# Kernel tuning notes

Measured on AMD Instinct MI355X. Metric: run time of the kernel, lower is better.

## Reference

```python
import jax, jax.numpy as jnp
import numpy as np

DIM = 128
G = 2
N = G * G * G
EPS = 1e-5


def _positions():
    pos = []
    for x in range(G):
        for y in range(G):
            for z in range(G):
                pos.append([x / (G - 1), y / (G - 1), z / (G - 1)])
    return np.asarray(pos, dtype=np.float32)  # [N, 3]


def _nearby(idx):
    x = idx // (G * G)
    y = (idx % (G * G)) // G
    z = idx % G
    nb = []
    for dx in (-1, 0, 1):
        for dy in (-1, 0, 1):
            for dz in (-1, 0, 1):
                nx, ny, nz = x + dx, y + dy, z + dz
                if 0 <= nx < G and 0 <= ny < G and 0 <= nz < G:
                    nidx = nx * G * G + ny * G + nz
                    if nidx != idx:
                        nb.append(nidx)
    return nb


def _ln(h, g, b):
    m = h.mean(-1, keepdims=True)
    v = ((h - m) ** 2).mean(-1, keepdims=True)
    return (h - m) * jax.lax.rsqrt(v + EPS) * g + b


def setup_inputs() -> dict:
    key = jax.random.key(0)
    ks = jax.random.split(key, 16)
    B = 131072
    f32 = jnp.float32
    return {
        "x": jax.random.normal(ks[0], (B, DIM), f32),
        "field_basis": jax.random.normal(ks[1], (N, 8, DIM), f32) * 0.02,
        "spatial_mix": jax.random.normal(ks[2], (N, 3, DIM), f32) * 0.02,
        "ln1_g": jnp.ones((N, DIM), f32),
        "ln1_b": jnp.zeros((N, DIM), f32),
        "w1": jax.random.normal(ks[3], (N, DIM, 2 * DIM), f32) * 0.02,
        "b1": jnp.zeros((N, 2 * DIM), f32),
        "w2": jax.random.normal(ks[4], (N, 2 * DIM, DIM), f32) * 0.02,
        "b2": jnp.zeros((N, DIM), f32),
        "ln2_g": jnp.ones((N, DIM), f32),
        "ln2_b": jnp.zeros((N, DIM), f32),
        "comb_ln_g": jnp.ones((DIM,), f32),
        "comb_ln_b": jnp.zeros((DIM,), f32),
        "comb_w": jax.random.normal(ks[5], (DIM, DIM), f32) * 0.02,
        "comb_b": jnp.zeros((DIM,), f32),
    }


def reference(x, field_basis, spatial_mix, ln1_g, ln1_b, w1, b1, w2, b2,
              ln2_g, ln2_b, comb_ln_g, comb_ln_b, comb_w, comb_b):
    pos = jnp.asarray(_positions())  # [N, 3] constant grid positions
    states = []
    for i in range(N):
        # per-module field value
        pw = jax.nn.sigmoid(pos[i] @ spatial_mix[i])          # [dim]
        fv = (field_basis[i] * pw).mean(0)                     # [dim]
        # neighbor contribution: only previously computed modules (j < i)
        nbrs = [j for j in _nearby(i) if j < i]
        h = x + fv
        if nbrs:
            nc = 0.1 * jnp.mean(jnp.stack([states[j] for j in nbrs], 0), 0)
            h = h + nc
        # LN -> Linear(dim,2dim) -> GELU(exact) -> Linear(2dim,dim) -> LN
        h = _ln(h, ln1_g[i], ln1_b[i])
        h = jax.nn.gelu(h @ w1[i] + b1[i], approximate=False)
        h = h @ w2[i] + b2[i]
        h = _ln(h, ln2_g[i], ln2_b[i])
        states.append(h)
    s = jnp.stack(states, 1).mean(1)                           # [B, dim]
    return _ln(s, comb_ln_g, comb_ln_b) @ comb_w + comb_b
```

## Files before the change

kernel.cpp:

```cpp
#include <hip/hip_runtime.h>
#include <math.h>


#define NMOD 8

typedef float    f32x4  __attribute__((ext_vector_type(4)));
typedef _Float16 f16x8  __attribute__((ext_vector_type(8)));
typedef _Float16 f16x2  __attribute__((ext_vector_type(2)));
typedef __fp16   fp16v2 __attribute__((ext_vector_type(2)));

union PKC { fp16v2 raw; f16x2 v; };
static __device__ __forceinline__ f16x2 pkrtz(float a, float b) {
    PKC u; u.raw = __builtin_amdgcn_cvt_pkrtz(a, b); return u.v;
}

union U16V { f16x8 v; f16x2 p[4]; };

#define AHI_OFF 0u
#define ALO_OFF 8192u
#define HHI_OFF 16384u
#define HLO_OFF 24576u

#define WS_W1 0u
#define WS_W2 1048576u
#define WS_CW 2097152u
#define WS_FV 2162688u

#define WSCALE 64.0f
#define INV64  0.015625f

static __device__ __forceinline__ float gelu_fast(float y) {
    float z  = y * 0.70710678118654752440f;
    float az = fabsf(z);
    float t  = __builtin_amdgcn_rcpf(1.0f + 0.3275911f * az);
    float poly = t * (0.254829592f + t * (-0.284496736f + t * (1.421413741f
               + t * (-1.453152027f + t * 1.061405429f))));
    float e  = __expf(-az * az);
    float erfa = 1.0f - poly * e;
    float er = (z < 0.0f) ? -erfa : erfa;
    return 0.5f * y * (1.0f + er);
}

#define MFMA16(a, b, c) __builtin_amdgcn_mfma_f32_16x16x32_f16((a), (b), (c), 0, 0, 0)

__global__ void setup_weights(const float* __restrict__ w1,
                              const float* __restrict__ w2,
                              const float* __restrict__ cw,
                              _Float16* __restrict__ w1cv,
                              _Float16* __restrict__ w2cv,
                              _Float16* __restrict__ cwcv)
{
    unsigned id = blockIdx.x * blockDim.x + threadIdx.x;
    if (id < 262144u) {
        unsigned i8 = id & 7u;
        unsigned l  = (id >> 3) & 63u;
        unsigned nt = (id >> 9) & 15u;
        unsigned ks = (id >> 13) & 3u;
        unsigned mo = id >> 15;
        unsigned k = ks * 32u + ((l >> 4) << 3) + i8;
        unsigned c = nt * 16u + (l & 15u);
        float v = w1[(mo * 128u + k) * 256u + c] * WSCALE;
        _Float16 hh = (_Float16)v;
        _Float16 ll = (_Float16)(v - (float)hh);
        w1cv[((((mo * 2u + 0u) * 4u + ks) * 16u + nt) * 64u + l) * 8u + i8] = hh;
        w1cv[((((mo * 2u + 1u) * 4u + ks) * 16u + nt) * 64u + l) * 8u + i8] = ll;
    } else if (id < 524288u) {
        unsigned id2 = id - 262144u;
        unsigned i8 = id2 & 7u;
        unsigned l  = (id2 >> 3) & 63u;
        unsigned nt = (id2 >> 9) & 7u;
        unsigned kt = (id2 >> 12) & 7u;
        unsigned mo = id2 >> 15;
        unsigned k = kt * 32u + ((l >> 4) << 3) + i8;
        unsigned c = nt * 16u + (l & 15u);
        float v = w2[(mo * 256u + k) * 128u + c] * WSCALE;
        _Float16 hh = (_Float16)v;
        _Float16 ll = (_Float16)(v - (float)hh);
        w2cv[((((mo * 2u + 0u) * 8u + kt) * 8u + nt) * 64u + l) * 8u + i8] = hh;
        w2cv[((((mo * 2u + 1u) * 8u + kt) * 8u + nt) * 64u + l) * 8u + i8] = ll;
    } else if (id < 540672u) {
        unsigned id3 = id - 524288u;
        unsigned i8 = id3 & 7u;
        unsigned l  = (id3 >> 3) & 63u;
        unsigned nt = (id3 >> 9) & 7u;
        unsigned ks = id3 >> 12;
        unsigned k = ks * 32u + ((l >> 4) << 3) + i8;
        unsigned c = nt * 16u + (l & 15u);
        float v = cw[k * 128u + c] * WSCALE;
        _Float16 hh = (_Float16)v;
        _Float16 ll = (_Float16)(v - (float)hh);
        cwcv[(((0u * 4u + ks) * 8u + nt) * 64u + l) * 8u + i8] = hh;
        cwcv[(((1u * 4u + ks) * 8u + nt) * 64u + l) * 8u + i8] = ll;
    }
}

__global__ void setup_fv(const float* __restrict__ fb,
                         const float* __restrict__ sm,
                         float* __restrict__ fv)
{
    unsigned tid = blockIdx.x * blockDim.x + threadIdx.x;
    unsigned i = tid >> 7, d = tid & 127u;
    float px = (float)((i >> 2) & 1u);
    float py = (float)((i >> 1) & 1u);
    float pz = (float)(i & 1u);
    float dot = px * sm[(i * 3u + 0u) * 128u + d]
              + py * sm[(i * 3u + 1u) * 128u + d]
              + pz * sm[(i * 3u + 2u) * 128u + d];
    float pw = 1.0f / (1.0f + expf(-dot));
    float mb = 0.0f;
    #pragma unroll
    for (int k = 0; k < 8; ++k) mb += fb[(i * 8u + (unsigned)k) * 128u + d];
    mb *= 0.125f;
    fv[i * 128u + d] = pw * mb;
}

__global__ __launch_bounds__(256)
__attribute__((amdgpu_waves_per_eu(3, 4)))
void holo_main(const float* __restrict__ x,
               const float* __restrict__ ln1_g, const float* __restrict__ ln1_b,
               const float* __restrict__ bias1, const float* __restrict__ bias2,
               const float* __restrict__ ln2_g, const float* __restrict__ ln2_b,
               const float* __restrict__ cln_g, const float* __restrict__ cln_b,
               const float* __restrict__ comb_b,
               const _Float16* __restrict__ w1cv,
               const _Float16* __restrict__ w2cv,
               const _Float16* __restrict__ cwcv,
               const float* __restrict__ fv,
               float* __restrict__ out)
{
    __shared__ __align__(16) unsigned char lds[32768];

    const unsigned t  = threadIdx.x;
    const unsigned r  = t >> 3;
    const unsigned q8 = t & 7u;
    const unsigned w  = t >> 6;
    const unsigned l  = t & 63u;
    const unsigned lr = l & 15u;
    const unsigned lg = l >> 4;
    const unsigned drow = lg * 4u;
    const unsigned row0 = blockIdx.x * 32u;

    const f32x4 FZ = {0.f, 0.f, 0.f, 0.f};

    float Sv[16];
    #pragma unroll
    for (int j = 0; j < 16; ++j) Sv[j] = 0.f;

    for (int mod = 0; mod < NMOD; ++mod) {
        const unsigned mo = (unsigned)mod;
        {
            const float coef = (mod == 0) ? 0.0f : (0.1f / (float)mod);
            float h[16];
            const float4* xp  = (const float4*)(x  + (row0 + r) * 128u + q8 * 16u);
            const float4* fvp = (const float4*)(fv + mo * 128u + q8 * 16u);
            #pragma unroll
            for (int u = 0; u < 4; ++u) {
                float4 xv = xp[u];
                float4 f4 = fvp[u];
                h[4*u+0] = xv.x + f4.x + coef * Sv[4*u+0];
                h[4*u+1] = xv.y + f4.y + coef * Sv[4*u+1];
                h[4*u+2] = xv.z + f4.z + coef * Sv[4*u+2];
                h[4*u+3] = xv.w + f4.w + coef * Sv[4*u+3];
            }
            float s = 0.f;
            #pragma unroll
            for (int j = 0; j < 16; ++j) s += h[j];
            s += __shfl_xor(s, 1); s += __shfl_xor(s, 2); s += __shfl_xor(s, 4);
            const float mean = s * (1.0f / 128.0f);
            float ss = 0.f;
            #pragma unroll
            for (int j = 0; j < 16; ++j) { float d = h[j] - mean; ss += d * d; }
            ss += __shfl_xor(ss, 1); ss += __shfl_xor(ss, 2); ss += __shfl_xor(ss, 4);
            const float var  = ss * (1.0f / 128.0f);
            const float rstd = 1.0f / sqrtf(var + 1e-5f);
            const float4* gp = (const float4*)(ln1_g + mo * 128u + q8 * 16u);
            const float4* bp = (const float4*)(ln1_b + mo * 128u + q8 * 16u);
            #pragma unroll
            for (int e2 = 0; e2 < 2; ++e2) {
                U16V vh, vl;
                #pragma unroll
                for (int u = 0; u < 2; ++u) {
                    float4 g4 = gp[e2*2+u], b4 = bp[e2*2+u];
                    int e0 = e2*8 + u*4;
                    float n0 = (h[e0+0] - mean) * rstd * g4.x + b4.x;
                    float n1 = (h[e0+1] - mean) * rstd * g4.y + b4.y;
                    float n2 = (h[e0+2] - mean) * rstd * g4.z + b4.z;
                    float n3 = (h[e0+3] - mean) * rstd * g4.w + b4.w;
                    f16x2 h01 = pkrtz(n0, n1);
                    f16x2 h23 = pkrtz(n2, n3);
                    f16x2 l01 = pkrtz(n0 - (float)h01[0], n1 - (float)h01[1]);
                    f16x2 l23 = pkrtz(n2 - (float)h23[0], n3 - (float)h23[1]);
                    vh.p[u*2+0] = h01; vh.p[u*2+1] = h23;
                    vl.p[u*2+0] = l01; vl.p[u*2+1] = l23;
                }
                unsigned off = ((r * 256u + q8 * 32u + (unsigned)e2 * 16u) ^ ((r & 7u) << 4));
                *(f16x8*)(lds + AHI_OFF + off) = vh.v;
                *(f16x8*)(lds + ALO_OFF + off) = vl.v;
            }
        }
        __syncthreads();

        f32x4 acc2[2][2];
        #pragma unroll
        for (int m = 0; m < 2; ++m) { acc2[m][0] = FZ; acc2[m][1] = FZ; }

        #pragma unroll
        for (int hN = 0; hN < 2; ++hN) {
            if (hN == 1) __syncthreads();
            #pragma unroll
            for (int n = 0; n < 2; ++n) {
                f32x4 a1[2];
                a1[0] = FZ; a1[1] = FZ;
                #pragma unroll
                for (int ks = 0; ks < 4; ++ks) {
                    f16x8 ah[2], al[2];
                    #pragma unroll
                    for (int m = 0; m < 2; ++m) {
                        unsigned rowA = (unsigned)m * 16u + lr;
                        unsigned off = ((rowA * 256u + (unsigned)ks * 64u + lg * 16u) ^ ((lr & 7u) << 4));
                        ah[m] = *(const f16x8*)(lds + AHI_OFF + off);
                        al[m] = *(const f16x8*)(lds + ALO_OFF + off);
                    }
                    unsigned ntg = (unsigned)hN * 8u + w * 2u + (unsigned)n;
                    const f16x8 bh = *(const f16x8*)(const void*)
                        (w1cv + (((mo * 2u + 0u) * 4u + (unsigned)ks) * 16u + ntg) * 512u + l * 8u);
                    const f16x8 bl = *(const f16x8*)(const void*)
                        (w1cv + (((mo * 2u + 1u) * 4u + (unsigned)ks) * 16u + ntg) * 512u + l * 8u);
                    #pragma unroll
                    for (int m = 0; m < 2; ++m) {
                        a1[m] = MFMA16(ah[m], bh, a1[m]);
                        a1[m] = MFMA16(al[m], bh, a1[m]);
                        a1[m] = MFMA16(ah[m], bl, a1[m]);
                    }
                }
                unsigned c128 = w * 32u + (unsigned)n * 16u + lr;
                float bb = bias1[mo * 256u + (unsigned)hN * 128u + c128];
                #pragma unroll
                for (int m = 0; m < 2; ++m) {
                    float ge[4];
                    #pragma unroll
                    for (int j = 0; j < 4; ++j)
                        ge[j] = gelu_fast(a1[m][j] * INV64 + bb);
                    f16x2 h01 = pkrtz(ge[0], ge[1]);
                    f16x2 h23 = pkrtz(ge[2], ge[3]);
                    f16x2 l01 = pkrtz(ge[0] - (float)h01[0], ge[1] - (float)h01[1]);
                    f16x2 l23 = pkrtz(ge[2] - (float)h23[0], ge[3] - (float)h23[1]);
                    _Float16 hv[4] = {h01[0], h01[1], h23[0], h23[1]};
                    _Float16 lv[4] = {l01[0], l01[1], l23[0], l23[1]};
                    #pragma unroll
                    for (int j = 0; j < 4; ++j) {
                        unsigned rowA = (unsigned)m * 16u + drow + (unsigned)j;
                        unsigned off = ((rowA * 256u + c128 * 2u) ^ ((rowA & 7u) << 4));
                        *(_Float16*)(lds + HHI_OFF + off) = hv[j];
                        *(_Float16*)(lds + HLO_OFF + off) = lv[j];
                    }
                }
            }
            __syncthreads();
            #pragma unroll
            for (int ks = 0; ks < 4; ++ks) {
                unsigned kt = (unsigned)hN * 4u + (unsigned)ks;
                f16x8 ah2[2], al2[2];
                #pragma unroll
                for (int m = 0; m < 2; ++m) {
                    unsigned rowA = (unsigned)m * 16u + lr;
                    unsigned off = ((rowA * 256u + (unsigned)ks * 64u + lg * 16u) ^ ((lr & 7u) << 4));
                    ah2[m] = *(const f16x8*)(lds + HHI_OFF + off);
                    al2[m] = *(const f16x8*)(lds + HLO_OFF + off);
                }
                #pragma unroll
                for (int n = 0; n < 2; ++n) {
                    unsigned nt2 = w * 2u + (unsigned)n;
                    const f16x8 bh = *(const f16x8*)(const void*)
                        (w2cv + (((mo * 2u + 0u) * 8u + kt) * 8u + nt2) * 512u + l * 8u);
                    const f16x8 bl = *(const f16x8*)(const void*)
                        (w2cv + (((mo * 2u + 1u) * 8u + kt) * 8u + nt2) * 512u + l * 8u);
                    #pragma unroll
                    for (int m = 0; m < 2; ++m) {
                        acc2[m][n] = MFMA16(ah2[m], bh, acc2[m][n]);
                        acc2[m][n] = MFMA16(al2[m], bh, acc2[m][n]);
                        acc2[m][n] = MFMA16(ah2[m], bl, acc2[m][n]);
                    }
                }
            }
        }
        #pragma unroll
        for (int n = 0; n < 2; ++n) {
            unsigned c = w * 32u + (unsigned)n * 16u + lr;
            float bb = bias2[mo * 128u + c];
            #pragma unroll
            for (int m = 0; m < 2; ++m) {
                #pragma unroll
                for (int j = 0; j < 4; ++j) {
                    unsigned rowA = (unsigned)m * 16u + drow + (unsigned)j;
                    unsigned off = ((rowA * 512u + c * 4u) ^ ((rowA & 7u) << 4));
                    *(float*)(lds + off) = acc2[m][n][j] * INV64 + bb;
                }
            }
        }
        __syncthreads();
        {
            float h2[16];
            #pragma unroll
            for (int e = 0; e < 4; ++e) {
                unsigned off = ((r * 512u + q8 * 64u + (unsigned)e * 16u) ^ ((r & 7u) << 4));
                float4 v = *(const float4*)(lds + off);
                h2[4*e+0] = v.x; h2[4*e+1] = v.y; h2[4*e+2] = v.z; h2[4*e+3] = v.w;
            }
            float s = 0.f;
            #pragma unroll
            for (int j = 0; j < 16; ++j) s += h2[j];
            s += __shfl_xor(s, 1); s += __shfl_xor(s, 2); s += __shfl_xor(s, 4);
            const float mean = s * (1.0f / 128.0f);
            float ss = 0.f;
            #pragma unroll
            for (int j = 0; j < 16; ++j) { float d = h2[j] - mean; ss += d * d; }
            ss += __shfl_xor(ss, 1); ss += __shfl_xor(ss, 2); ss += __shfl_xor(ss, 4);
            const float var  = ss * (1.0f / 128.0f);
            const float rstd = 1.0f / sqrtf(var + 1e-5f);
            const float4* gp = (const float4*)(ln2_g + mo * 128u + q8 * 16u);
            const float4* bp = (const float4*)(ln2_b + mo * 128u + q8 * 16u);
            #pragma unroll
            for (int u = 0; u < 4; ++u) {
                float4 g4 = gp[u], b4 = bp[u];
                Sv[4*u+0] += (h2[4*u+0] - mean) * rstd * g4.x + b4.x;
                Sv[4*u+1] += (h2[4*u+1] - mean) * rstd * g4.y + b4.y;
                Sv[4*u+2] += (h2[4*u+2] - mean) * rstd * g4.z + b4.z;
                Sv[4*u+3] += (h2[4*u+3] - mean) * rstd * g4.w + b4.w;
            }
        }
        __syncthreads();
    }

    {
        float h[16];
        #pragma unroll
        for (int j = 0; j < 16; ++j) h[j] = Sv[j] * 0.125f;
        float s = 0.f;
        #pragma unroll
        for (int j = 0; j < 16; ++j) s += h[j];
        s += __shfl_xor(s, 1); s += __shfl_xor(s, 2); s += __shfl_xor(s, 4);
        const float mean = s * (1.0f / 128.0f);
        float ss = 0.f;
        #pragma unroll
        for (int j = 0; j < 16; ++j) { float d = h[j] - mean; ss += d * d; }
        ss += __shfl_xor(ss, 1); ss += __shfl_xor(ss, 2); ss += __shfl_xor(ss, 4);
        const float var  = ss * (1.0f / 128.0f);
        const float rstd = 1.0f / sqrtf(var + 1e-5f);
        const float4* gp = (const float4*)(cln_g + q8 * 16u);
        const float4* bp = (const float4*)(cln_b + q8 * 16u);
        #pragma unroll
        for (int e2 = 0; e2 < 2; ++e2) {
            U16V vh, vl;
            #pragma unroll
            for (int u = 0; u < 2; ++u) {
                float4 g4 = gp[e2*2+u], b4 = bp[e2*2+u];
                int e0 = e2*8 + u*4;
                float n0 = (h[e0+0] - mean) * rstd * g4.x + b4.x;
                float n1 = (h[e0+1] - mean) * rstd * g4.y + b4.y;
                float n2 = (h[e0+2] - mean) * rstd * g4.z + b4.z;
                float n3 = (h[e0+3] - mean) * rstd * g4.w + b4.w;
                f16x2 h01 = pkrtz(n0, n1);
                f16x2 h23 = pkrtz(n2, n3);
                f16x2 l01 = pkrtz(n0 - (float)h01[0], n1 - (float)h01[1]);
                f16x2 l23 = pkrtz(n2 - (float)h23[0], n3 - (float)h23[1]);
                vh.p[u*2+0] = h01; vh.p[u*2+1] = h23;
                vl.p[u*2+0] = l01; vl.p[u*2+1] = l23;
            }
            unsigned off = ((r * 256u + q8 * 32u + (unsigned)e2 * 16u) ^ ((r & 7u) << 4));
            *(f16x8*)(lds + AHI_OFF + off) = vh.v;
            *(f16x8*)(lds + ALO_OFF + off) = vl.v;
        }
    }
    __syncthreads();
    {
        #pragma unroll
        for (int n = 0; n < 2; ++n) {
            f32x4 a3[2];
            a3[0] = FZ; a3[1] = FZ;
            #pragma unroll
            for (int ks = 0; ks < 4; ++ks) {
                f16x8 ah[2], al[2];
                #pragma unroll
                for (int m = 0; m < 2; ++m) {
                    unsigned rowA = (unsigned)m * 16u + lr;
                    unsigned off = ((rowA * 256u + (unsigned)ks * 64u + lg * 16u) ^ ((lr & 7u) << 4));
                    ah[m] = *(const f16x8*)(lds + AHI_OFF + off);
                    al[m] = *(const f16x8*)(lds + ALO_OFF + off);
                }
                unsigned nt = w * 2u + (unsigned)n;
                const f16x8 bh = *(const f16x8*)(const void*)
                    (cwcv + ((0u * 4u + (unsigned)ks) * 8u + nt) * 512u + l * 8u);
                const f16x8 bl = *(const f16x8*)(const void*)
                    (cwcv + ((1u * 4u + (unsigned)ks) * 8u + nt) * 512u + l * 8u);
                #pragma unroll
                for (int m = 0; m < 2; ++m) {
                    a3[m] = MFMA16(ah[m], bh, a3[m]);
                    a3[m] = MFMA16(al[m], bh, a3[m]);
                    a3[m] = MFMA16(ah[m], bl, a3[m]);
                }
            }
            unsigned col = w * 32u + (unsigned)n * 16u + lr;
            float bb = comb_b[col];
            #pragma unroll
            for (int m = 0; m < 2; ++m) {
                #pragma unroll
                for (int j = 0; j < 4; ++j) {
                    unsigned rowA = (unsigned)m * 16u + drow + (unsigned)j;
                    out[(row0 + rowA) * 128u + col] = a3[m][j] * INV64 + bb;
                }
            }
        }
    }
}

extern "C" void kernel_launch(void* const* d_in, const int* in_sizes, int n_in,
                              void* d_out, int out_size, void* d_ws, size_t ws_size,
                              hipStream_t stream)
{
    const float* x    = (const float*)d_in[0];
    const float* fb   = (const float*)d_in[1];
    const float* sm   = (const float*)d_in[2];
    const float* ln1g = (const float*)d_in[3];
    const float* ln1b = (const float*)d_in[4];
    const float* w1   = (const float*)d_in[5];
    const float* b1   = (const float*)d_in[6];
    const float* w2   = (const float*)d_in[7];
    const float* b2   = (const float*)d_in[8];
    const float* ln2g = (const float*)d_in[9];
    const float* ln2b = (const float*)d_in[10];
    const float* clng = (const float*)d_in[11];
    const float* clnb = (const float*)d_in[12];
    const float* cw   = (const float*)d_in[13];
    const float* cb   = (const float*)d_in[14];
    float* out = (float*)d_out;
    char* ws = (char*)d_ws;
    _Float16* w1cv = (_Float16*)(ws + WS_W1);
    _Float16* w2cv = (_Float16*)(ws + WS_W2);
    _Float16* cwcv = (_Float16*)(ws + WS_CW);
    float*    fvp  = (float*)(ws + WS_FV);

    setup_weights<<<dim3(2112), dim3(256), 0, stream>>>(w1, w2, cw, w1cv, w2cv, cwcv);
    setup_fv<<<dim3(4), dim3(256), 0, stream>>>(fb, sm, fvp);
    holo_main<<<dim3(4096), dim3(256), 0, stream>>>(x, ln1g, ln1b, b1, b2, ln2g, ln2b,
                                                    clng, clnb, cb, w1cv, w2cv, cwcv, fvp, out);
    (void)in_sizes; (void)n_in; (void)out_size; (void)ws_size;
}
```

Baseline: 725.4 us.

## Double-buffer GELU hidden tiles in LDS to cut barriers and cache x in registers

Splits the hidden activation staging into two LDS buffers (H0/H1), so the second half of GEMM1 can be written while GEMM2 reads the first half. This removes two of the per-module __syncthreads. It also loads x once into registers instead of reloading it from global memory for each of the 8 modules, and moves the LN2 staging area so the trailing barrier can be dropped. LDS use grows from 32 KB to 48 KB per block and the extra 16 registers for x raise register pressure, which could lower occupancy.

```diff
diff --git a/kernel.cpp b/kernel.cpp
--- a/kernel.cpp
+++ b/kernel.cpp
@@ -16,10 +16,13 @@
 
 union U16V { f16x8 v; f16x2 p[4]; };
 
-#define AHI_OFF 0u
-#define ALO_OFF 8192u
-#define HHI_OFF 16384u
-#define HLO_OFF 24576u
+#define AHI_OFF  0u
+#define ALO_OFF  8192u
+#define H0HI_OFF 16384u
+#define H0LO_OFF 24576u
+#define H1HI_OFF 32768u
+#define H1LO_OFF 40960u
+#define ST_OFF   16384u
 
 #define WS_W1 0u
 #define WS_W2 1048576u
@@ -128,7 +131,7 @@
                const float* __restrict__ fv,
                float* __restrict__ out)
 {
-    __shared__ __align__(16) unsigned char lds[32768];
+    __shared__ __align__(16) unsigned char lds[49152];
 
     const unsigned t  = threadIdx.x;
     const unsigned r  = t >> 3;
@@ -142,25 +145,31 @@
 
     const f32x4 FZ = {0.f, 0.f, 0.f, 0.f};
 
-    float Sv[16];
+    float Sv[16], xv[16];
     #pragma unroll
     for (int j = 0; j < 16; ++j) Sv[j] = 0.f;
+    {
+        const float4* xp = (const float4*)(x + (row0 + r) * 128u + q8 * 16u);
+        #pragma unroll
+        for (int u = 0; u < 4; ++u) {
+            float4 v = xp[u];
+            xv[4*u+0] = v.x; xv[4*u+1] = v.y; xv[4*u+2] = v.z; xv[4*u+3] = v.w;
+        }
+    }
 
     for (int mod = 0; mod < NMOD; ++mod) {
         const unsigned mo = (unsigned)mod;
         {
             const float coef = (mod == 0) ? 0.0f : (0.1f / (float)mod);
             float h[16];
-            const float4* xp  = (const float4*)(x  + (row0 + r) * 128u + q8 * 16u);
             const float4* fvp = (const float4*)(fv + mo * 128u + q8 * 16u);
             #pragma unroll
             for (int u = 0; u < 4; ++u) {
-                float4 xv = xp[u];
                 float4 f4 = fvp[u];
-                h[4*u+0] = xv.x + f4.x + coef * Sv[4*u+0];
-                h[4*u+1] = xv.y + f4.y + coef * Sv[4*u+1];
-                h[4*u+2] = xv.z + f4.z + coef * Sv[4*u+2];
-                h[4*u+3] = xv.w + f4.w + coef * Sv[4*u+3];
+                h[4*u+0] = xv[4*u+0] + f4.x + coef * Sv[4*u+0];
+                h[4*u+1] = xv[4*u+1] + f4.y + coef * Sv[4*u+1];
+                h[4*u+2] = xv[4*u+2] + f4.z + coef * Sv[4*u+2];
+                h[4*u+3] = xv[4*u+3] + f4.w + coef * Sv[4*u+3];
             }
             float s = 0.f;
             #pragma unroll
@@ -205,82 +214,156 @@
         for (int m = 0; m < 2; ++m) { acc2[m][0] = FZ; acc2[m][1] = FZ; }
 
         #pragma unroll
-        for (int hN = 0; hN < 2; ++hN) {
-            if (hN == 1) __syncthreads();
-            #pragma unroll
-            for (int n = 0; n < 2; ++n) {
-                f32x4 a1[2];
-                a1[0] = FZ; a1[1] = FZ;
-                #pragma unroll
-                for (int ks = 0; ks < 4; ++ks) {
-                    f16x8 ah[2], al[2];
-                    #pragma unroll
-                    for (int m = 0; m < 2; ++m) {
-                        unsigned rowA = (unsigned)m * 16u + lr;
-                        unsigned off = ((rowA * 256u + (unsigned)ks * 64u + lg * 16u) ^ ((lr & 7u) << 4));
-                        ah[m] = *(const f16x8*)(lds + AHI_OFF + off);
-                        al[m] = *(const f16x8*)(lds + ALO_OFF + off);
-                    }
-                    unsigned ntg = (unsigned)hN * 8u + w * 2u + (unsigned)n;
-                    const f16x8 bh = *(const f16x8*)(const void*)
-                        (w1cv + (((mo * 2u + 0u) * 4u + (unsigned)ks) * 16u + ntg) * 512u + l * 8u);
-                    const f16x8 bl = *(const f16x8*)(const void*)
-                        (w1cv + (((mo * 2u + 1u) * 4u + (unsigned)ks) * 16u + ntg) * 512u + l * 8u);
-                    #pragma unroll
-                    for (int m = 0; m < 2; ++m) {
-                        a1[m] = MFMA16(ah[m], bh, a1[m]);
-                        a1[m] = MFMA16(al[m], bh, a1[m]);
-                        a1[m] = MFMA16(ah[m], bl, a1[m]);
-                    }
-                }
-                unsigned c128 = w * 32u + (unsigned)n * 16u + lr;
-                float bb = bias1[mo * 256u + (unsigned)hN * 128u + c128];
-                #pragma unroll
-                for (int m = 0; m < 2; ++m) {
-                    float ge[4];
-                    #pragma unroll
-                    for (int j = 0; j < 4; ++j)
-                        ge[j] = gelu_fast(a1[m][j] * INV64 + bb);
-                    f16x2 h01 = pkrtz(ge[0], ge[1]);
-                    f16x2 h23 = pkrtz(ge[2], ge[3]);
-                    f16x2 l01 = pkrtz(ge[0] - (float)h01[0], ge[1] - (float)h01[1]);
-                    f16x2 l23 = pkrtz(ge[2] - (float)h23[0], ge[3] - (float)h23[1]);
-                    _Float16 hv[4] = {h01[0], h01[1], h23[0], h23[1]};
-                    _Float16 lv[4] = {l01[0], l01[1], l23[0], l23[1]};
-                    #pragma unroll
-                    for (int j = 0; j < 4; ++j) {
-                        unsigned rowA = (unsigned)m * 16u + drow + (unsigned)j;
-                        unsigned off = ((rowA * 256u + c128 * 2u) ^ ((rowA & 7u) << 4));
-                        *(_Float16*)(lds + HHI_OFF + off) = hv[j];
-                        *(_Float16*)(lds + HLO_OFF + off) = lv[j];
-                    }
-                }
-            }
-            __syncthreads();
+        for (int n = 0; n < 2; ++n) {
+            f32x4 a1[2];
+            a1[0] = FZ; a1[1] = FZ;
             #pragma unroll
             for (int ks = 0; ks < 4; ++ks) {
-                unsigned kt = (unsigned)hN * 4u + (unsigned)ks;
-                f16x8 ah2[2], al2[2];
+                f16x8 ah[2], al[2];
                 #pragma unroll
                 for (int m = 0; m < 2; ++m) {
                     unsigned rowA = (unsigned)m * 16u + lr;
                     unsigned off = ((rowA * 256u + (unsigned)ks * 64u + lg * 16u) ^ ((lr & 7u) << 4));
-                    ah2[m] = *(const f16x8*)(lds + HHI_OFF + off);
-                    al2[m] = *(const f16x8*)(lds + HLO_OFF + off);
-                }
-                #pragma unroll
-                for (int n = 0; n < 2; ++n) {
-                    unsigned nt2 = w * 2u + (unsigned)n;
-                    const f16x8 bh = *(const f16x8*)(const void*)
-                        (w2cv + (((mo * 2u + 0u) * 8u + kt) * 8u + nt2) * 512u + l * 8u);
-                    const f16x8 bl = *(const f16x8*)(const void*)
-                        (w2cv + (((mo * 2u + 1u) * 8u + kt) * 8u + nt2) * 512u + l * 8u);
-                    #pragma unroll
-                    for (int m = 0; m < 2; ++m) {
-                        acc2[m][n] = MFMA16(ah2[m], bh, acc2[m][n]);
-                        acc2[m][n] = MFMA16(al2[m], bh, acc2[m][n]);
-                        acc2[m][n] = MFMA16(ah2[m], bl, acc2[m][n]);
-                    }
+                    ah[m] = *(const f16x8*)(lds + AHI_OFF + off);
+                    al[m] = *(const f16x8*)(lds + ALO_OFF + off);
+                }
+                unsigned ntg = w * 2u + (unsigned)n;
+                const f16x8 bh = *(const f16x8*)(const void*)
+                    (w1cv + (((mo * 2u + 0u) * 4u + (unsigned)ks) * 16u + ntg) * 512u + l * 8u);
+                const f16x8 bl = *(const f16x8*)(const void*)
+                    (w1cv + (((mo * 2u + 1u) * 4u + (unsigned)ks) * 16u + ntg) * 512u + l * 8u);
+                #pragma unroll
+                for (int m = 0; m < 2; ++m) {
+                    a1[m] = MFMA16(ah[m], bh, a1[m]);
+                    a1[m] = MFMA16(al[m], bh, a1[m]);
+                    a1[m] = MFMA16(ah[m], bl, a1[m]);
+                }
+            }
+            unsigned c128 = w * 32u + (unsigned)n * 16u + lr;
+            float bb = bias1[mo * 256u + c128];
+            #pragma unroll
+            for (int m = 0; m < 2; ++m) {
+                float ge[4];
+                #pragma unroll
+                for (int j = 0; j < 4; ++j)
+                    ge[j] = gelu_fast(a1[m][j] * INV64 + bb);
+                f16x2 h01 = pkrtz(ge[0], ge[1]);
+                f16x2 h23 = pkrtz(ge[2], ge[3]);
+                f16x2 l01 = pkrtz(ge[0] - (float)h01[0], ge[1] - (float)h01[1]);
+                f16x2 l23 = pkrtz(ge[2] - (float)h23[0], ge[3] - (float)h23[1]);
+                _Float16 hv[4] = {h01[0], h01[1], h23[0], h23[1]};
+                _Float16 lv[4] = {l01[0], l01[1], l23[0], l23[1]};
+                #pragma unroll
+                for (int j = 0; j < 4; ++j) {
+                    unsigned rowA = (unsigned)m * 16u + drow + (unsigned)j;
+                    unsigned off = ((rowA * 256u + c128 * 2u) ^ ((rowA & 7u) << 4));
+                    *(_Float16*)(lds + H0HI_OFF + off) = hv[j];
+                    *(_Float16*)(lds + H0LO_OFF + off) = lv[j];
+                }
+            }
+        }
+        __syncthreads();
+
+        #pragma unroll
+        for (int n = 0; n < 2; ++n) {
+            f32x4 a1[2];
+            a1[0] = FZ; a1[1] = FZ;
+            #pragma unroll
+            for (int ks = 0; ks < 4; ++ks) {
+                f16x8 ah[2], al[2];
+                #pragma unroll
+                for (int m = 0; m < 2; ++m) {
+                    unsigned rowA = (unsigned)m * 16u + lr;
+                    unsigned off = ((rowA * 256u + (unsigned)ks * 64u + lg * 16u) ^ ((lr & 7u) << 4));
+                    ah[m] = *(const f16x8*)(lds + AHI_OFF + off);
+                    al[m] = *(const f16x8*)(lds + ALO_OFF + off);
+                }
+                unsigned ntg = 8u + w * 2u + (unsigned)n;
+                const f16x8 bh = *(const f16x8*)(const void*)
+                    (w1cv + (((mo * 2u + 0u) * 4u + (unsigned)ks) * 16u + ntg) * 512u + l * 8u);
+                const f16x8 bl = *(const f16x8*)(const void*)
+                    (w1cv + (((mo * 2u + 1u) * 4u + (unsigned)ks) * 16u + ntg) * 512u + l * 8u);
+                #pragma unroll
+                for (int m = 0; m < 2; ++m) {
+                    a1[m] = MFMA16(ah[m], bh, a1[m]);
+                    a1[m] = MFMA16(al[m], bh, a1[m]);
+                    a1[m] = MFMA16(ah[m], bl, a1[m]);
+                }
+            }
+            unsigned c128 = w * 32u + (unsigned)n * 16u + lr;
+            float bb = bias1[mo * 256u + 128u + c128];
+            #pragma unroll
+            for (int m = 0; m < 2; ++m) {
+                float ge[4];
+                #pragma unroll
+                for (int j = 0; j < 4; ++j)
+                    ge[j] = gelu_fast(a1[m][j] * INV64 + bb);
+                f16x2 h01 = pkrtz(ge[0], ge[1]);
+                f16x2 h23 = pkrtz(ge[2], ge[3]);
+                f16x2 l01 = pkrtz(ge[0] - (float)h01[0], ge[1] - (float)h01[1]);
+                f16x2 l23 = pkrtz(ge[2] - (float)h23[0], ge[3] - (float)h23[1]);
+                _Float16 hv[4] = {h01[0], h01[1], h23[0], h23[1]};
+                _Float16 lv[4] = {l01[0], l01[1], l23[0], l23[1]};
+                #pragma unroll
+                for (int j = 0; j < 4; ++j) {
+                    unsigned rowA = (unsigned)m * 16u + drow + (unsigned)j;
+                    unsigned off = ((rowA * 256u + c128 * 2u) ^ ((rowA & 7u) << 4));
+                    *(_Float16*)(lds + H1HI_OFF + off) = hv[j];
+                    *(_Float16*)(lds + H1LO_OFF + off) = lv[j];
+                }
+            }
+        }
+        #pragma unroll
+        for (int ks = 0; ks < 4; ++ks) {
+            unsigned kt = (unsigned)ks;
+            f16x8 ah2[2], al2[2];
+            #pragma unroll
+            for (int m = 0; m < 2; ++m) {
+                unsigned rowA = (unsigned)m * 16u + lr;
+                unsigned off = ((rowA * 256u + (unsigned)ks * 64u + lg * 16u) ^ ((lr & 7u) << 4));
+                ah2[m] = *(const f16x8*)(lds + H0HI_OFF + off);
+                al2[m] = *(const f16x8*)(lds + H0LO_OFF + off);
+            }
+            #pragma unroll
+            for (int n = 0; n < 2; ++n) {
+                unsigned nt2 = w * 2u + (unsigned)n;
+                const f16x8 bh = *(const f16x8*)(const void*)
+                    (w2cv + (((mo * 2u + 0u) * 8u + kt) * 8u + nt2) * 512u + l * 8u);
+                const f16x8 bl = *(const f16x8*)(const void*)
+                    (w2cv + (((mo * 2u + 1u) * 8u + kt) * 8u + nt2) * 512u + l * 8u);
+                #pragma unroll
+                for (int m = 0; m < 2; ++m) {
+                    acc2[m][n] = MFMA16(ah2[m], bh, acc2[m][n]);
+                    acc2[m][n] = MFMA16(al2[m], bh, acc2[m][n]);
+                    acc2[m][n] = MFMA16(ah2[m], bl, acc2[m][n]);
+                }
+            }
+        }
+        __syncthreads();
+
+        #pragma unroll
+        for (int ks = 0; ks < 4; ++ks) {
+            unsigned kt = 4u + (unsigned)ks;
+            f16x8 ah2[2], al2[2];
+            #pragma unroll
+            for (int m = 0; m < 2; ++m) {
+                unsigned rowA = (unsigned)m * 16u + lr;
+                unsigned off = ((rowA * 256u + (unsigned)ks * 64u + lg * 16u) ^ ((lr & 7u) << 4));
+                ah2[m] = *(const f16x8*)(lds + H1HI_OFF + off);
+                al2[m] = *(const f16x8*)(lds + H1LO_OFF + off);
+            }
+            #pragma unroll
+            for (int n = 0; n < 2; ++n) {
+                unsigned nt2 = w * 2u + (unsigned)n;
+                const f16x8 bh = *(const f16x8*)(const void*)
+                    (w2cv + (((mo * 2u + 0u) * 8u + kt) * 8u + nt2) * 512u + l * 8u);
+                const f16x8 bl = *(const f16x8*)(const void*)
+                    (w2cv + (((mo * 2u + 1u) * 8u + kt) * 8u + nt2) * 512u + l * 8u);
+                #pragma unroll
+                for (int m = 0; m < 2; ++m) {
+                    acc2[m][n] = MFMA16(ah2[m], bh, acc2[m][n]);
+                    acc2[m][n] = MFMA16(al2[m], bh, acc2[m][n]);
+                    acc2[m][n] = MFMA16(ah2[m], bl, acc2[m][n]);
                 }
             }
         }
@@ -294,17 +377,18 @@
                 for (int j = 0; j < 4; ++j) {
                     unsigned rowA = (unsigned)m * 16u + drow + (unsigned)j;
                     unsigned off = ((rowA * 512u + c * 4u) ^ ((rowA & 7u) << 4));
-                    *(float*)(lds + off) = acc2[m][n][j] * INV64 + bb;
+                    *(float*)(lds + ST_OFF + off) = acc2[m][n][j] * INV64 + bb;
                 }
             }
         }
         __syncthreads();
+
         {
             float h2[16];
             #pragma unroll
             for (int e = 0; e < 4; ++e) {
                 unsigned off = ((r * 512u + q8 * 64u + (unsigned)e * 16u) ^ ((r & 7u) << 4));
-                float4 v = *(const float4*)(lds + off);
+                float4 v = *(const float4*)(lds + ST_OFF + off);
                 h2[4*e+0] = v.x; h2[4*e+1] = v.y; h2[4*e+2] = v.z; h2[4*e+3] = v.w;
             }
             float s = 0.f;
@@ -329,7 +413,6 @@
                 Sv[4*u+3] += (h2[4*u+3] - mean) * rstd * g4.w + b4.w;
             }
         }
-        __syncthreads();
     }
 
     {
```

Result: faster. 678.0 us, median of 2 (-6.5%).
